# Optimization experiments

Hardware: AMD Instinct MI355X
Metric: run time of the kernel (lower is better)

## Reference

```python
import jax, jax.numpy as jnp
import numpy as np

EPS = 1e-5
NUM_GROUPS = 8


def setup_inputs() -> dict:
    key = jax.random.key(0)
    ks = jax.random.split(key, 8)
    B, C, H, W = 4, 64, 64, 64
    scale_w = 1.0 / np.sqrt(C)  # roughly xavier scale for [C,C]
    return {
        "x": jax.random.normal(ks[0], (B, C, H, W), dtype=jnp.float32),
        "gamma": jnp.ones((C,), dtype=jnp.float32),
        "beta": jnp.zeros((C,), dtype=jnp.float32),
        "Wq": jax.random.normal(ks[1], (C, C), dtype=jnp.float32) * scale_w,
        "bq": jnp.zeros((C,), dtype=jnp.float32),
        "Wk": jax.random.normal(ks[2], (C, C), dtype=jnp.float32) * scale_w,
        "bk": jnp.zeros((C,), dtype=jnp.float32),
        "Wv": jax.random.normal(ks[3], (C, C), dtype=jnp.float32) * scale_w,
        "bv": jnp.zeros((C,), dtype=jnp.float32),
        "Wp": jax.random.normal(ks[4], (C, C), dtype=jnp.float32) * scale_w,
        "bp": jnp.zeros((C,), dtype=jnp.float32),
    }


def _group_norm(x, gamma, beta):
    # x: [B, C, H, W]; normalize over (C//G, H, W) within each of G groups
    B, C, H, W = x.shape
    xg = x.reshape(B, NUM_GROUPS, -1)
    mean = jnp.mean(xg, axis=-1, keepdims=True)
    var = jnp.var(xg, axis=-1, keepdims=True)
    xn = ((xg - mean) * jax.lax.rsqrt(var + EPS)).reshape(B, C, H, W)
    return xn * gamma[None, :, None, None] + beta[None, :, None, None]


def reference(x, gamma, beta, Wq, bq, Wk, bk, Wv, bv, Wp, bp):
    B, C, H, W = x.shape
    N = H * W
    xn = _group_norm(x, gamma, beta).reshape(B, C, N)  # [B, C, N]
    # 1x1 convs == per-pixel linear maps over channels
    q = jnp.einsum('oc,bcn->bon', Wq, xn) + bq[None, :, None]  # [B, C, N]
    k = jnp.einsum('oc,bcn->bon', Wk, xn) + bk[None, :, None]
    v = jnp.einsum('oc,bcn->bon', Wv, xn) + bv[None, :, None]
    scale = 1.0 / jnp.sqrt(jnp.asarray(C, dtype=x.dtype))
    attn = jnp.einsum('bcn,bcm->bnm', q, k) * scale  # [B, N, N]
    attn = jax.nn.softmax(attn, axis=-1)
    out = jnp.einsum('bnm,bcm->bcn', attn, v)  # [B, C, N]
    out = jnp.einsum('oc,bcn->bon', Wp, out) + bp[None, :, None]
    return x + out.reshape(B, C, H, W)
```

## Files before the change

### kernel.cpp

```cpp
#include <hip/hip_runtime.h>
#include <math.h>

#define B_ 4
#define C_ 64
#define N_ 4096

typedef unsigned short u16;
typedef __attribute__((ext_vector_type(8))) short bf16x8;
typedef __attribute__((ext_vector_type(4))) float f32x4;

__device__ __forceinline__ u16 f2bf(float f) {
    unsigned u = __float_as_uint(f);
    u += 0x7fff + ((u >> 16) & 1);
    return (u16)(u >> 16);
}
__device__ __forceinline__ float bf2f(u16 h) {
    return __uint_as_float(((unsigned)h) << 16);
}

__global__ __launch_bounds__(256) void gn_reduce(const float* __restrict__ x,
                                                 float* __restrict__ partials) {
    int bg = blockIdx.x >> 3, chunk = blockIdx.x & 7;
    const float4* xv = (const float4*)(x + (size_t)bg * 32768 + (size_t)chunk * 4096);
    float s = 0.f, ss = 0.f;
    #pragma unroll
    for (int k = 0; k < 4; k++) {
        float4 v = xv[threadIdx.x + 256 * k];
        s += v.x + v.y + v.z + v.w;
        ss += v.x * v.x + v.y * v.y + v.z * v.z + v.w * v.w;
    }
    #pragma unroll
    for (int off = 1; off < 64; off <<= 1) {
        s += __shfl_xor(s, off);
        ss += __shfl_xor(ss, off);
    }
    __shared__ float red[2][4];
    int w = threadIdx.x >> 6;
    if ((threadIdx.x & 63) == 0) { red[0][w] = s; red[1][w] = ss; }
    __syncthreads();
    if (threadIdx.x == 0) {
        s = red[0][0] + red[0][1] + red[0][2] + red[0][3];
        ss = red[1][0] + red[1][1] + red[1][2] + red[1][3];
        partials[bg * 16 + chunk * 2] = s;
        partials[bg * 16 + chunk * 2 + 1] = ss;
    }
}

__global__ __launch_bounds__(256) void qkv_kernel(
    const float* __restrict__ x, const float* __restrict__ gamma,
    const float* __restrict__ beta, const float* __restrict__ partials,
    const float* __restrict__ Wq, const float* __restrict__ bq,
    const float* __restrict__ Wk, const float* __restrict__ bk,
    const float* __restrict__ Wv, const float* __restrict__ bv,
    u16* __restrict__ Qo, u16* __restrict__ Ko, u16* __restrict__ Vt) {
    __shared__ __align__(16) u16 wt[3][64][64];
    __shared__ __align__(16) u16 xs[64][64];
    __shared__ __align__(16) u16 odt[64][72];

    const int b = blockIdx.x >> 6;
    const int nt = blockIdx.x & 63;
    const int tid = threadIdx.x;
    const float* Ws[3] = {Wq, Wk, Wv};
    const float* bs[3] = {bq, bk, bv};

    {
        const int rw = tid >> 2, qd = tid & 3;
        #pragma unroll
        for (int s = 0; s < 3; s++) {
            const float4* wsrc = (const float4*)(Ws[s] + rw * 64 + qd * 16);
            float4 f0 = wsrc[0], f1 = wsrc[1], f2 = wsrc[2], f3 = wsrc[3];
            u16 pk[16];
            pk[0]=f2bf(f0.x); pk[1]=f2bf(f0.y); pk[2]=f2bf(f0.z); pk[3]=f2bf(f0.w);
            pk[4]=f2bf(f1.x); pk[5]=f2bf(f1.y); pk[6]=f2bf(f1.z); pk[7]=f2bf(f1.w);
            pk[8]=f2bf(f2.x); pk[9]=f2bf(f2.y); pk[10]=f2bf(f2.z); pk[11]=f2bf(f2.w);
            pk[12]=f2bf(f3.x); pk[13]=f2bf(f3.y); pk[14]=f2bf(f3.z); pk[15]=f2bf(f3.w);
            int blk0 = (2 * qd) ^ (rw & 7), blk1 = (2 * qd + 1) ^ (rw & 7);
            *(uint4*)&wt[s][rw][blk0 * 8] = *(uint4*)&pk[0];
            *(uint4*)&wt[s][rw][blk1 * 8] = *(uint4*)&pk[8];
        }
    }
    {
        const int c = tid >> 2, px0 = (tid & 3) * 16;
        const int g = c >> 3, bg = b * 8 + g;
        float s = 0.f, ss = 0.f;
        #pragma unroll
        for (int i = 0; i < 8; i++) {
            s += partials[bg * 16 + i * 2];
            ss += partials[bg * 16 + i * 2 + 1];
        }
        float mean = s * (1.f / 32768.f);
        float var = ss * (1.f / 32768.f) - mean * mean;
        float rstd = rsqrtf(var + 1e-5f);
        float ga = gamma[c] * rstd;
        float bb = beta[c] - mean * ga;
        const float4* xp = (const float4*)(x + ((size_t)(b * 64 + c)) * N_ + nt * 64 + px0);
        float4 q0 = xp[0], q1 = xp[1], q2 = xp[2], q3 = xp[3];
        float vals[16] = {q0.x,q0.y,q0.z,q0.w, q1.x,q1.y,q1.z,q1.w,
                          q2.x,q2.y,q2.z,q2.w, q3.x,q3.y,q3.z,q3.w};
        #pragma unroll
        for (int e = 0; e < 16; e++) {
            int px = px0 + e;
            xs[px][((c >> 3) ^ (px & 7)) * 8 + (c & 7)] = f2bf(vals[e] * ga + bb);
        }
    }
    __syncthreads();

    const int lane = tid & 63, w = tid >> 6;
    const int lr = lane & 15, lg = lane >> 4;
    const f32x4 zz = {0.f, 0.f, 0.f, 0.f};
    const int sa0 = (lg ^ (lr & 7)) * 8, sa1 = ((4 | lg) ^ (lr & 7)) * 8;

    #pragma unroll
    for (int s = 0; s < 3; s++) {
        bf16x8 a0 = *(const bf16x8*)&wt[s][w * 16 + lr][sa0];
        bf16x8 a1 = *(const bf16x8*)&wt[s][w * 16 + lr][sa1];
        float bias[4];
        #pragma unroll
        for (int r = 0; r < 4; r++) bias[r] = bs[s][w * 16 + lg * 4 + r];
        #pragma unroll
        for (int pt = 0; pt < 4; pt++) {
            bf16x8 b0 = *(const bf16x8*)&xs[pt * 16 + lr][sa0];
            bf16x8 b1 = *(const bf16x8*)&xs[pt * 16 + lr][sa1];
            f32x4 acc = __builtin_amdgcn_mfma_f32_16x16x32_bf16(a0, b0, zz, 0, 0, 0);
            acc = __builtin_amdgcn_mfma_f32_16x16x32_bf16(a1, b1, acc, 0, 0, 0);
            if (s == 0) {
                #pragma unroll
                for (int r = 0; r < 4; r++)
                    odt[pt * 16 + lr][w * 16 + lg * 4 + r] = f2bf((acc[r] + bias[r]) * 0.18033688f);
            } else if (s == 1) {
                #pragma unroll
                for (int r = 0; r < 4; r++)
                    odt[pt * 16 + lr][w * 16 + lg * 4 + r] = f2bf(acc[r] + bias[r]);
            } else {
                #pragma unroll
                for (int r = 0; r < 4; r++)
                    odt[w * 16 + lg * 4 + r][pt * 16 + lr] = f2bf(acc[r] + bias[r]);
            }
        }
        __syncthreads();
        if (s < 2) {
            u16* dst = (s == 0 ? Qo : Ko) + ((size_t)(b * N_ + nt * 64)) * 64;
            #pragma unroll
            for (int k2 = 0; k2 < 2; k2++) {
                int c = tid + k2 * 256;
                int px = c >> 3, blk = c & 7;
                *(uint4*)(dst + (size_t)px * 64 + blk * 8) = *(const uint4*)&odt[px][blk * 8];
            }
        } else {
            #pragma unroll
            for (int k2 = 0; k2 < 2; k2++) {
                int c = tid + k2 * 256;
                int co = c >> 3, blk = c & 7;
                *(uint4*)(Vt + ((size_t)(b * 64 + co)) * N_ + nt * 64 + blk * 8) =
                    *(const uint4*)&odt[co][blk * 8];
            }
        }
        __syncthreads();
    }
}

__global__ __launch_bounds__(256) void flash_kernel(
    const u16* __restrict__ Qg, const u16* __restrict__ Kg,
    const u16* __restrict__ Vg, u16* __restrict__ Opart, float* __restrict__ ml,
    int nsplit) {
    __shared__ __align__(16) u16 Ks[2][4096];
    __shared__ __align__(16) u16 Vs[2][5120];
    __shared__ __align__(16) u16 Ps[4][1024];

    const int sp = blockIdx.x >> 8;
    const int b  = (blockIdx.x >> 6) & 3;
    const int qt = blockIdx.x & 63;
    const int tid = threadIdx.x;
    const int w = tid >> 6, lane = tid & 63;
    const int lr = lane & 15, lg = lane >> 4;

    const int per = (nsplit == 3) ? 22 : 32;
    const int kt0 = sp * per;
    const int NT = min(per, 64 - kt0);

    for (int i = tid; i < 2048; i += 256) {
        int bufi = i >> 10, off = i & 1023;
        Vs[bufi][4096 + off] = (off < 64) ? (u16)0x3F80 : (u16)0;
    }

    const u16* qrow = Qg + ((size_t)(b * N_ + qt * 64 + w * 16 + lr)) * C_;
    bf16x8 aq0 = *(const bf16x8*)(qrow + lg * 8);
    bf16x8 aq1 = *(const bf16x8*)(qrow + 32 + lg * 8);

    const int srow = tid >> 2;
    const int scb  = (tid & 3) * 32;
    const char* Kbase = (const char*)(Kg + (size_t)b * N_ * C_) + (size_t)srow * 128 + scb;
    const char* Vbase = (const char*)(Vg + (size_t)b * C_ * N_) + (size_t)srow * (N_ * 2) + scb;
    const int se0 = srow * 64 + (((scb)      ^ ((srow & 7) << 4)) >> 1);
    const int se1 = srow * 64 + (((scb + 16) ^ ((srow & 7) << 4)) >> 1);

    const int sw0 = ((lg ^ (lr & 7)) << 3);
    const int sw1 = (((4 | lg) ^ (lr & 7)) << 3);

    u16* pswr[4][4];
    #pragma unroll
    for (int r = 0; r < 4; r++) {
        int q = lg * 4 + r, sz = (q & 7) << 3;
        #pragma unroll
        for (int ct = 0; ct < 4; ct++)
            pswr[r][ct] = &Ps[w][q * 64 + ((ct * 16 + lr) ^ sz)];
    }

    {
        uint4 k0a = *(const uint4*)(Kbase + (size_t)kt0 * 8192);
        uint4 k0b = *(const uint4*)(Kbase + (size_t)kt0 * 8192 + 16);
        uint4 v0a = *(const uint4*)(Vbase + kt0 * 128);
        uint4 v0b = *(const uint4*)(Vbase + kt0 * 128 + 16);
        *(uint4*)&Ks[0][se0] = k0a;  *(uint4*)&Ks[0][se1] = k0b;
        *(uint4*)&Vs[0][se0] = v0a;  *(uint4*)&Vs[0][se1] = v0b;
    }
    uint4 ka = *(const uint4*)(Kbase + (size_t)(kt0 + 1) * 8192);
    uint4 kb = *(const uint4*)(Kbase + (size_t)(kt0 + 1) * 8192 + 16);
    uint4 va = *(const uint4*)(Vbase + (kt0 + 1) * 128);
    uint4 vb = *(const uint4*)(Vbase + (kt0 + 1) * 128 + 16);
    __syncthreads();

    f32x4 zz = {0.f, 0.f, 0.f, 0.f};
    f32x4 o[5];
    #pragma unroll
    for (int ct = 0; ct < 5; ct++) o[ct] = zz;

    auto body = [&](int t, int bi) {
        const u16* ks = Ks[bi];
        const u16* vs = Vs[bi];

        f32x4 s[4];
        __builtin_amdgcn_s_setprio(1);
        #pragma unroll
        for (int ct = 0; ct < 4; ct++) {
            bf16x8 b0 = *(const bf16x8*)&ks[(ct * 16 + lr) * 64 + sw0];
            bf16x8 b1 = *(const bf16x8*)&ks[(ct * 16 + lr) * 64 + sw1];
            f32x4 acc = __builtin_amdgcn_mfma_f32_16x16x32_bf16(aq0, b0, zz, 0, 0, 0);
            acc = __builtin_amdgcn_mfma_f32_16x16x32_bf16(aq1, b1, acc, 0, 0, 0);
            s[ct] = acc;
        }
        __builtin_amdgcn_s_setprio(0);

        #pragma unroll
        for (int r = 0; r < 4; r++) {
            float p0 = exp2f(s[0][r] - 12.f);
            float p1 = exp2f(s[1][r] - 12.f);
            float p2 = exp2f(s[2][r] - 12.f);
            float p3 = exp2f(s[3][r] - 12.f);
            unsigned pk0, pk1;
            asm("v_cvt_pk_bf16_f32 %0, %1, %2" : "=v"(pk0) : "v"(p0), "v"(p1));
            asm("v_cvt_pk_bf16_f32 %0, %1, %2" : "=v"(pk1) : "v"(p2), "v"(p3));
            *pswr[r][0] = (u16)pk0;
            *pswr[r][1] = (u16)(pk0 >> 16);
            *pswr[r][2] = (u16)pk1;
            *pswr[r][3] = (u16)(pk1 >> 16);
        }
        asm volatile("s_waitcnt lgkmcnt(0)" ::: "memory");

        __builtin_amdgcn_s_setprio(1);
        #pragma unroll
        for (int kk = 0; kk < 2; kk++) {
            const int sw = kk ? sw1 : sw0;
            bf16x8 pa = *(const bf16x8*)&Ps[w][lr * 64 + sw];
            #pragma unroll
            for (int ct = 0; ct < 5; ct++) {
                bf16x8 bv = *(const bf16x8*)&vs[(ct * 16 + lr) * 64 + sw];
                o[ct] = __builtin_amdgcn_mfma_f32_16x16x32_bf16(pa, bv, o[ct], 0, 0, 0);
            }
        }
        __builtin_amdgcn_s_setprio(0);

        if (t < NT - 1) {
            u16* kd = Ks[bi ^ 1];
            u16* vd = Vs[bi ^ 1];
            *(uint4*)&kd[se0] = ka;  *(uint4*)&kd[se1] = kb;
            *(uint4*)&vd[se0] = va;  *(uint4*)&vd[se1] = vb;
        }
        __syncthreads();
        if (t < NT - 2) {
            int kt = kt0 + t + 2;
            ka = *(const uint4*)(Kbase + (size_t)kt * 8192);
            kb = *(const uint4*)(Kbase + (size_t)kt * 8192 + 16);
            va = *(const uint4*)(Vbase + kt * 128);
            vb = *(const uint4*)(Vbase + kt * 128 + 16);
        }
    };
    for (int tt = 0; tt < NT; tt += 2) { body(tt, 0); body(tt + 1, 1); }

    u16* op = Opart + (size_t)sp * 1048576
            + ((size_t)(b * N_ + qt * 64 + w * 16)) * C_;
    #pragma unroll
    for (int r = 0; r < 4; r++)
        #pragma unroll
        for (int ct = 0; ct < 4; ct++)
            op[(lg * 4 + r) * C_ + ct * 16 + lr] = f2bf(o[ct][r]);
    if (lr == 0) {
        float* mlp = ml + (size_t)sp * 16384 + b * N_ + qt * 64 + w * 16 + lg * 4;
        #pragma unroll
        for (int r = 0; r < 4; r++) mlp[r] = o[4][r];
    }
}

__global__ __launch_bounds__(256) void proj_kernel(
    const u16* __restrict__ Opart, const float* __restrict__ ml,
    const float* __restrict__ Wp, const float* __restrict__ bp,
    const float* __restrict__ x, float* __restrict__ out, int nsplit) {
    __shared__ __align__(16) u16 wp[64][64];
    __shared__ __align__(16) u16 og[64][64];
    const int b = blockIdx.x >> 6;
    const int nt = blockIdx.x & 63;
    const int tid = threadIdx.x;

    {
        const int rw = tid >> 2, qd = tid & 3;
        const float4* wsrc = (const float4*)(Wp + rw * 64 + qd * 16);
        float4 f0 = wsrc[0], f1 = wsrc[1], f2 = wsrc[2], f3 = wsrc[3];
        u16 pk[16];
        pk[0]=f2bf(f0.x); pk[1]=f2bf(f0.y); pk[2]=f2bf(f0.z); pk[3]=f2bf(f0.w);
        pk[4]=f2bf(f1.x); pk[5]=f2bf(f1.y); pk[6]=f2bf(f1.z); pk[7]=f2bf(f1.w);
        pk[8]=f2bf(f2.x); pk[9]=f2bf(f2.y); pk[10]=f2bf(f2.z); pk[11]=f2bf(f2.w);
        pk[12]=f2bf(f3.x); pk[13]=f2bf(f3.y); pk[14]=f2bf(f3.z); pk[15]=f2bf(f3.w);
        int blk0 = (2 * qd) ^ (rw & 7), blk1 = (2 * qd + 1) ^ (rw & 7);
        *(uint4*)&wp[rw][blk0 * 8] = *(uint4*)&pk[0];
        *(uint4*)&wp[rw][blk1 * 8] = *(uint4*)&pk[8];
    }
    {
        #pragma unroll
        for (int k2 = 0; k2 < 2; k2++) {
            int cidx = tid + k2 * 256;
            int px = cidx >> 3, blk = cidx & 7;
            int gpix = b * N_ + nt * 64 + px;
            float lsum = 0.f;
            for (int s = 0; s < nsplit; s++) lsum += ml[(size_t)s * 16384 + gpix];
            float inv = 1.f / lsum;
            float acc8[8] = {0.f,0.f,0.f,0.f,0.f,0.f,0.f,0.f};
            for (int s = 0; s < nsplit; s++) {
                u16 ov[8];
                *(uint4*)ov = *(const uint4*)(Opart + (size_t)s * 1048576 + (size_t)gpix * 64 + blk * 8);
                #pragma unroll
                for (int j = 0; j < 8; j++) acc8[j] += bf2f(ov[j]);
            }
            u16 y[8];
            #pragma unroll
            for (int j = 0; j < 8; j++) y[j] = f2bf(acc8[j] * inv);
            *(uint4*)&og[px][(blk ^ (px & 7)) * 8] = *(uint4*)y;
        }
    }
    __syncthreads();

    const int lane = tid & 63, w = tid >> 6;
    const int lr = lane & 15, lg = lane >> 4;
    const f32x4 zz = {0.f, 0.f, 0.f, 0.f};
    const int sa0 = (lg ^ (lr & 7)) * 8, sa1 = ((4 | lg) ^ (lr & 7)) * 8;

    bf16x8 a0 = *(const bf16x8*)&wp[w * 16 + lr][sa0];
    bf16x8 a1 = *(const bf16x8*)&wp[w * 16 + lr][sa1];
    float bias[4];
    #pragma unroll
    for (int r = 0; r < 4; r++) bias[r] = bp[w * 16 + lg * 4 + r];

    #pragma unroll
    for (int pt = 0; pt < 4; pt++) {
        bf16x8 b0 = *(const bf16x8*)&og[pt * 16 + lr][sa0];
        bf16x8 b1 = *(const bf16x8*)&og[pt * 16 + lr][sa1];
        f32x4 acc = __builtin_amdgcn_mfma_f32_16x16x32_bf16(a0, b0, zz, 0, 0, 0);
        acc = __builtin_amdgcn_mfma_f32_16x16x32_bf16(a1, b1, acc, 0, 0, 0);
        #pragma unroll
        for (int r = 0; r < 4; r++) {
            int cout = w * 16 + lg * 4 + r;
            int px = pt * 16 + lr;
            size_t idx = ((size_t)(b * 64 + cout)) * N_ + nt * 64 + px;
            out[idx] = x[idx] + bias[r] + acc[r];
        }
    }
}

extern "C" void kernel_launch(void* const* d_in, const int* in_sizes, int n_in,
                              void* d_out, int out_size, void* d_ws, size_t ws_size,
                              hipStream_t stream) {
    const float* x     = (const float*)d_in[0];
    const float* gamma = (const float*)d_in[1];
    const float* beta  = (const float*)d_in[2];
    const float* Wq    = (const float*)d_in[3];
    const float* bq    = (const float*)d_in[4];
    const float* Wk    = (const float*)d_in[5];
    const float* bk    = (const float*)d_in[6];
    const float* Wv    = (const float*)d_in[7];
    const float* bv    = (const float*)d_in[8];
    const float* Wp    = (const float*)d_in[9];
    const float* bp    = (const float*)d_in[10];
    float* out = (float*)d_out;

    const size_t elems = (size_t)B_ * N_ * C_;
    float* partials = (float*)d_ws;
    float* ml = (float*)((char*)d_ws + 4096);
    u16* Qb = (u16*)((char*)d_ws + 4096 + 196608);
    u16* Kb = Qb + elems;
    u16* Vt = Kb + elems;
    u16* Opart = Vt + elems;

    const size_t need3 = 4096 + 196608 + 3 * elems * 2 + 3 * elems * 2;
    const int nsplit = (ws_size >= need3) ? 3 : 2;

    gn_reduce<<<256, 256, 0, stream>>>(x, partials);
    qkv_kernel<<<256, 256, 0, stream>>>(x, gamma, beta, partials,
                                        Wq, bq, Wk, bk, Wv, bv, Qb, Kb, Vt);
    flash_kernel<<<nsplit * 256, 256, 0, stream>>>(Qb, Kb, Vt, Opart, ml, nsplit);
    proj_kernel<<<256, 256, 0, stream>>>(Opart, ml, Wp, bp, x, out, nsplit);
}
```

Before: 58.60 us.

## Switch flash kernel to 32x32 MFMA with register-resident P and key split

The attention kernel now uses 32x32x16 bf16 MFMAs. The P tile is repacked in registers via permlane32_swap instead of a round trip through shared memory, and the row sum is accumulated directly rather than through an extra ones-column in V. Each of the four waves takes a 32-query by 32-key slice, and partial outputs are reduced across wave pairs through LDS at the end. Shared memory is smaller, launch bounds request 4 blocks per CU, and the key split can now go to 4 when workspace allows, adding parallelism. The risks are a larger accumulator register footprint, the extra end-of-kernel reduction and sync, and more partial outputs for the projection kernel to combine.

```diff
diff --git a/kernel.cpp b/kernel.cpp
--- a/kernel.cpp
+++ b/kernel.cpp
@@ -8,6 +8,8 @@
 typedef unsigned short u16;
 typedef __attribute__((ext_vector_type(8))) short bf16x8;
 typedef __attribute__((ext_vector_type(4))) float f32x4;
+typedef __attribute__((ext_vector_type(16))) float f32x16;
+typedef __attribute__((ext_vector_type(2))) int i32x2;
 
 __device__ __forceinline__ u16 f2bf(float f) {
     unsigned u = __float_as_uint(f);
@@ -159,33 +161,33 @@
     }
 }
 
-__global__ __launch_bounds__(256) void flash_kernel(
+__global__ __launch_bounds__(256, 4) void flash_kernel(
     const u16* __restrict__ Qg, const u16* __restrict__ Kg,
     const u16* __restrict__ Vg, u16* __restrict__ Opart, float* __restrict__ ml,
     int nsplit) {
-    __shared__ __align__(16) u16 Ks[2][4096];
-    __shared__ __align__(16) u16 Vs[2][5120];
-    __shared__ __align__(16) u16 Ps[4][1024];
+    __shared__ __align__(16) u16 smem[16384];
+    u16* const Ksb0 = smem;
+    u16* const Ksb1 = smem + 4096;
+    u16* const Vsb0 = smem + 8192;
+    u16* const Vsb1 = smem + 12288;
 
     const int sp = blockIdx.x >> 8;
     const int b  = (blockIdx.x >> 6) & 3;
     const int qt = blockIdx.x & 63;
     const int tid = threadIdx.x;
     const int w = tid >> 6, lane = tid & 63;
-    const int lr = lane & 15, lg = lane >> 4;
-
-    const int per = (nsplit == 3) ? 22 : 32;
+    const int l31 = lane & 31, lh = lane >> 5;
+    const int qh = w >> 1, kh = w & 1;
+
+    const int per = (nsplit == 4) ? 16 : (nsplit == 3) ? 22 : 32;
     const int kt0 = sp * per;
     const int NT = min(per, 64 - kt0);
 
-    for (int i = tid; i < 2048; i += 256) {
-        int bufi = i >> 10, off = i & 1023;
-        Vs[bufi][4096 + off] = (off < 64) ? (u16)0x3F80 : (u16)0;
-    }
-
-    const u16* qrow = Qg + ((size_t)(b * N_ + qt * 64 + w * 16 + lr)) * C_;
-    bf16x8 aq0 = *(const bf16x8*)(qrow + lg * 8);
-    bf16x8 aq1 = *(const bf16x8*)(qrow + 32 + lg * 8);
+    const u16* qptr = Qg + ((size_t)(b * N_ + qt * 64 + qh * 32 + l31)) * 64 + lh * 8;
+    bf16x8 q0 = *(const bf16x8*)(qptr);
+    bf16x8 q1 = *(const bf16x8*)(qptr + 16);
+    bf16x8 q2 = *(const bf16x8*)(qptr + 32);
+    bf16x8 q3 = *(const bf16x8*)(qptr + 48);
 
     const int srow = tid >> 2;
     const int scb  = (tid & 3) * 32;
@@ -194,16 +196,18 @@
     const int se0 = srow * 64 + (((scb)      ^ ((srow & 7) << 4)) >> 1);
     const int se1 = srow * 64 + (((scb + 16) ^ ((srow & 7) << 4)) >> 1);
 
-    const int sw0 = ((lg ^ (lr & 7)) << 3);
-    const int sw1 = (((4 | lg) ^ (lr & 7)) << 3);
-
-    u16* pswr[4][4];
-    #pragma unroll
-    for (int r = 0; r < 4; r++) {
-        int q = lg * 4 + r, sz = (q & 7) << 3;
-        #pragma unroll
-        for (int ct = 0; ct < 4; ct++)
-            pswr[r][ct] = &Ps[w][q * 64 + ((ct * 16 + lr) ^ sz)];
+    const int key = kh * 32 + l31;
+    int kaoff[4];
+    #pragma unroll
+    for (int s = 0; s < 4; s++)
+        kaoff[s] = key * 64 + (((s * 2 + lh) ^ (key & 7)) << 3);
+    int vboff[2][2];
+    #pragma unroll
+    for (int c = 0; c < 2; c++) {
+        int ch = c * 32 + l31;
+        #pragma unroll
+        for (int s = 0; s < 2; s++)
+            vboff[c][s] = ch * 64 + (((kh * 4 + s * 2 + lh) ^ (ch & 7)) << 3);
     }
 
     {
@@ -211,8 +215,8 @@
         uint4 k0b = *(const uint4*)(Kbase + (size_t)kt0 * 8192 + 16);
         uint4 v0a = *(const uint4*)(Vbase + kt0 * 128);
         uint4 v0b = *(const uint4*)(Vbase + kt0 * 128 + 16);
-        *(uint4*)&Ks[0][se0] = k0a;  *(uint4*)&Ks[0][se1] = k0b;
-        *(uint4*)&Vs[0][se0] = v0a;  *(uint4*)&Vs[0][se1] = v0b;
+        *(uint4*)&Ksb0[se0] = k0a;  *(uint4*)&Ksb0[se1] = k0b;
+        *(uint4*)&Vsb0[se0] = v0a;  *(uint4*)&Vsb0[se1] = v0b;
     }
     uint4 ka = *(const uint4*)(Kbase + (size_t)(kt0 + 1) * 8192);
     uint4 kb = *(const uint4*)(Kbase + (size_t)(kt0 + 1) * 8192 + 16);
@@ -220,59 +224,58 @@
     uint4 vb = *(const uint4*)(Vbase + (kt0 + 1) * 128 + 16);
     __syncthreads();
 
-    f32x4 zz = {0.f, 0.f, 0.f, 0.f};
-    f32x4 o[5];
-    #pragma unroll
-    for (int ct = 0; ct < 5; ct++) o[ct] = zz;
+    f32x16 o0, o1;
+    #pragma unroll
+    for (int r = 0; r < 16; r++) { o0[r] = 0.f; o1[r] = 0.f; }
+    float lsum = 0.f;
 
     auto body = [&](int t, int bi) {
-        const u16* ks = Ks[bi];
-        const u16* vs = Vs[bi];
-
-        f32x4 s[4];
+        const u16* ks = bi ? Ksb1 : Ksb0;
+        const u16* vs = bi ? Vsb1 : Vsb0;
+        u16* kd = bi ? Ksb0 : Ksb1;
+        u16* vd = bi ? Vsb0 : Vsb1;
+
+        f32x16 st;
+        #pragma unroll
+        for (int r = 0; r < 16; r++) st[r] = 0.f;
         __builtin_amdgcn_s_setprio(1);
-        #pragma unroll
-        for (int ct = 0; ct < 4; ct++) {
-            bf16x8 b0 = *(const bf16x8*)&ks[(ct * 16 + lr) * 64 + sw0];
-            bf16x8 b1 = *(const bf16x8*)&ks[(ct * 16 + lr) * 64 + sw1];
-            f32x4 acc = __builtin_amdgcn_mfma_f32_16x16x32_bf16(aq0, b0, zz, 0, 0, 0);
-            acc = __builtin_amdgcn_mfma_f32_16x16x32_bf16(aq1, b1, acc, 0, 0, 0);
-            s[ct] = acc;
-        }
+        st = __builtin_amdgcn_mfma_f32_32x32x16_bf16(*(const bf16x8*)&ks[kaoff[0]], q0, st, 0, 0, 0);
+        st = __builtin_amdgcn_mfma_f32_32x32x16_bf16(*(const bf16x8*)&ks[kaoff[1]], q1, st, 0, 0, 0);
+        st = __builtin_amdgcn_mfma_f32_32x32x16_bf16(*(const bf16x8*)&ks[kaoff[2]], q2, st, 0, 0, 0);
+        st = __builtin_amdgcn_mfma_f32_32x32x16_bf16(*(const bf16x8*)&ks[kaoff[3]], q3, st, 0, 0, 0);
         __builtin_amdgcn_s_setprio(0);
 
-        #pragma unroll
-        for (int r = 0; r < 4; r++) {
-            float p0 = exp2f(s[0][r] - 12.f);
-            float p1 = exp2f(s[1][r] - 12.f);
-            float p2 = exp2f(s[2][r] - 12.f);
-            float p3 = exp2f(s[3][r] - 12.f);
-            unsigned pk0, pk1;
-            asm("v_cvt_pk_bf16_f32 %0, %1, %2" : "=v"(pk0) : "v"(p0), "v"(p1));
-            asm("v_cvt_pk_bf16_f32 %0, %1, %2" : "=v"(pk1) : "v"(p2), "v"(p3));
-            *pswr[r][0] = (u16)pk0;
-            *pswr[r][1] = (u16)(pk0 >> 16);
-            *pswr[r][2] = (u16)pk1;
-            *pswr[r][3] = (u16)(pk1 >> 16);
-        }
-        asm volatile("s_waitcnt lgkmcnt(0)" ::: "memory");
+        float p[16];
+        #pragma unroll
+        for (int r = 0; r < 16; r++) p[r] = exp2f(st[r] - 12.f);
+        lsum += (((p[0]+p[1])+(p[2]+p[3])) + ((p[4]+p[5])+(p[6]+p[7])))
+              + (((p[8]+p[9])+(p[10]+p[11])) + ((p[12]+p[13])+(p[14]+p[15])));
+
+        unsigned c0,c1,c2,c3,c4,c5,c6,c7;
+        asm("v_cvt_pk_bf16_f32 %0, %1, %2" : "=v"(c0) : "v"(p[0]),  "v"(p[1]));
+        asm("v_cvt_pk_bf16_f32 %0, %1, %2" : "=v"(c1) : "v"(p[2]),  "v"(p[3]));
+        asm("v_cvt_pk_bf16_f32 %0, %1, %2" : "=v"(c2) : "v"(p[4]),  "v"(p[5]));
+        asm("v_cvt_pk_bf16_f32 %0, %1, %2" : "=v"(c3) : "v"(p[6]),  "v"(p[7]));
+        asm("v_cvt_pk_bf16_f32 %0, %1, %2" : "=v"(c4) : "v"(p[8]),  "v"(p[9]));
+        asm("v_cvt_pk_bf16_f32 %0, %1, %2" : "=v"(c5) : "v"(p[10]), "v"(p[11]));
+        asm("v_cvt_pk_bf16_f32 %0, %1, %2" : "=v"(c6) : "v"(p[12]), "v"(p[13]));
+        asm("v_cvt_pk_bf16_f32 %0, %1, %2" : "=v"(c7) : "v"(p[14]), "v"(p[15]));
+        i32x2 r02 = __builtin_amdgcn_permlane32_swap((int)c0, (int)c2, false, false);
+        i32x2 r13 = __builtin_amdgcn_permlane32_swap((int)c1, (int)c3, false, false);
+        i32x2 r46 = __builtin_amdgcn_permlane32_swap((int)c4, (int)c6, false, false);
+        i32x2 r57 = __builtin_amdgcn_permlane32_swap((int)c5, (int)c7, false, false);
+        union U { int u[4]; bf16x8 v; };
+        U pa0 = {{r02[0], r13[0], r02[1], r13[1]}};
+        U pa1 = {{r46[0], r57[0], r46[1], r57[1]}};
 
         __builtin_amdgcn_s_setprio(1);
-        #pragma unroll
-        for (int kk = 0; kk < 2; kk++) {
-            const int sw = kk ? sw1 : sw0;
-            bf16x8 pa = *(const bf16x8*)&Ps[w][lr * 64 + sw];
-            #pragma unroll
-            for (int ct = 0; ct < 5; ct++) {
-                bf16x8 bv = *(const bf16x8*)&vs[(ct * 16 + lr) * 64 + sw];
-                o[ct] = __builtin_amdgcn_mfma_f32_16x16x32_bf16(pa, bv, o[ct], 0, 0, 0);
-            }
-        }
+        o0 = __builtin_amdgcn_mfma_f32_32x32x16_bf16(pa0.v, *(const bf16x8*)&vs[vboff[0][0]], o0, 0, 0, 0);
+        o0 = __builtin_amdgcn_mfma_f32_32x32x16_bf16(pa1.v, *(const bf16x8*)&vs[vboff[0][1]], o0, 0, 0, 0);
+        o1 = __builtin_amdgcn_mfma_f32_32x32x16_bf16(pa0.v, *(const bf16x8*)&vs[vboff[1][0]], o1, 0, 0, 0);
+        o1 = __builtin_amdgcn_mfma_f32_32x32x16_bf16(pa1.v, *(const bf16x8*)&vs[vboff[1][1]], o1, 0, 0, 0);
         __builtin_amdgcn_s_setprio(0);
 
         if (t < NT - 1) {
-            u16* kd = Ks[bi ^ 1];
-            u16* vd = Vs[bi ^ 1];
             *(uint4*)&kd[se0] = ka;  *(uint4*)&kd[se1] = kb;
             *(uint4*)&vd[se0] = va;  *(uint4*)&vd[se1] = vb;
         }
@@ -287,18 +290,37 @@
     };
     for (int tt = 0; tt < NT; tt += 2) { body(tt, 0); body(tt + 1, 1); }
 
-    u16* op = Opart + (size_t)sp * 1048576
-            + ((size_t)(b * N_ + qt * 64 + w * 16)) * C_;
-    #pragma unroll
-    for (int r = 0; r < 4; r++)
-        #pragma unroll
-        for (int ct = 0; ct < 4; ct++)
-            op[(lg * 4 + r) * C_ + ct * 16 + lr] = f2bf(o[ct][r]);
-    if (lr == 0) {
-        float* mlp = ml + (size_t)sp * 16384 + b * N_ + qt * 64 + w * 16 + lg * 4;
-        #pragma unroll
-        for (int r = 0; r < 4; r++) mlp[r] = o[4][r];
-    }
+    float* red = (float*)smem;
+    u16* ost = smem + 10240;
+    if (kh == 1) {
+        float* dst = red + (qh * 64 + lane) * 34;
+        #pragma unroll
+        for (int r = 0; r < 16; r++) { dst[r] = o0[r]; dst[16 + r] = o1[r]; }
+        dst[32] = lsum;
+    }
+    __syncthreads();
+    if (kh == 0) {
+        const float* src = red + (qh * 64 + lane) * 34;
+        float l2 = lsum + src[32];
+        i32x2 rr = __builtin_amdgcn_permlane32_swap(__float_as_int(l2), __float_as_int(l2), false, false);
+        float lpart = __int_as_float(lh ? rr[0] : rr[1]);
+        float lfull = l2 + lpart;
+        #pragma unroll
+        for (int r = 0; r < 16; r++) {
+            float v0 = o0[r] + src[r];
+            float v1 = o1[r] + src[16 + r];
+            int ql = qh * 32 + (r & 3) + 8 * (r >> 2) + 4 * lh;
+            ost[ql * 64 + l31] = f2bf(v0);
+            ost[ql * 64 + 32 + l31] = f2bf(v1);
+        }
+        if (lane < 32)
+            ml[(size_t)sp * 16384 + b * N_ + qt * 64 + qh * 32 + l31] = lfull;
+    }
+    __syncthreads();
+    uint4* op = (uint4*)(Opart + (size_t)sp * 1048576 + ((size_t)(b * N_ + qt * 64)) * 64);
+    const uint4* os4 = (const uint4*)ost;
+    op[tid] = os4[tid];
+    op[tid + 256] = os4[tid + 256];
 }
 
 __global__ __launch_bounds__(256) void proj_kernel(
@@ -392,15 +414,17 @@
     float* out = (float*)d_out;
 
     const size_t elems = (size_t)B_ * N_ * C_;
+    const size_t base = 4096 + 262144;
     float* partials = (float*)d_ws;
     float* ml = (float*)((char*)d_ws + 4096);
-    u16* Qb = (u16*)((char*)d_ws + 4096 + 196608);
+    u16* Qb = (u16*)((char*)d_ws + base);
     u16* Kb = Qb + elems;
     u16* Vt = Kb + elems;
     u16* Opart = Vt + elems;
 
-    const size_t need3 = 4096 + 196608 + 3 * elems * 2 + 3 * elems * 2;
-    const int nsplit = (ws_size >= need3) ? 3 : 2;
+    const size_t need4 = base + 3 * elems * 2 + 4 * elems * 2;
+    const size_t need3 = base + 3 * elems * 2 + 3 * elems * 2;
+    const int nsplit = (ws_size >= need4) ? 4 : (ws_size >= need3) ? 3 : 2;
 
     gn_reduce<<<256, 256, 0, stream>>>(x, partials);
     qkv_kernel<<<256, 256, 0, stream>>>(x, gamma, beta, partials,
```

Result: faster. 54.66 us (-6.7%).
